# Performance work log

Measured on AMD Instinct MI355X. Metric: run time of the kernel, lower is better.

## Reference

```python
import jax, jax.numpy as jnp
import numpy as np

SEQ, BATCH, EMBED = 2048, 4, 1024
NUM_HEADS = 16
HEAD_DIM = EMBED // NUM_HEADS


def setup_inputs() -> dict:
    key = jax.random.key(0)
    k1, k2, k3 = jax.random.split(key, 3)
    # xavier-ish scaling for weights
    query = jax.random.normal(k1, (SEQ, BATCH, EMBED), dtype=jnp.float32)
    in_proj_weight = jax.random.normal(k2, (3 * EMBED, EMBED), dtype=jnp.float32) * (2.0 / np.sqrt(EMBED + 3 * EMBED))
    out_proj_weight = jax.random.normal(k3, (EMBED, EMBED), dtype=jnp.float32) * (1.0 / np.sqrt(EMBED))
    in_proj_bias = jnp.zeros((3 * EMBED,), dtype=jnp.float32)
    out_proj_bias = jnp.zeros((EMBED,), dtype=jnp.float32)
    return {
        "query": query,
        "in_proj_weight": in_proj_weight,
        "in_proj_bias": in_proj_bias,
        "out_proj_weight": out_proj_weight,
        "out_proj_bias": out_proj_bias,
    }


def reference(query, in_proj_weight, in_proj_bias, out_proj_weight, out_proj_bias):
    T, B, C = query.shape
    H, D = NUM_HEADS, HEAD_DIM
    scaling = 1.0 / jnp.sqrt(jnp.asarray(D, dtype=query.dtype))
    # fused QKV projection: [T,B,C] @ [C,3C] -> [T,B,3C]
    qkv = query @ in_proj_weight.T + in_proj_bias
    q, k, v = jnp.split(qkv, 3, axis=-1)
    q = (q * scaling).reshape(T, B, H, D)
    k = k.reshape(T, B, H, D)
    v = v.reshape(T, B, H, D)
    # scores: [B,H,T,S]
    scores = jnp.einsum("tbhd,sbhd->bhts", q, k)
    probs = jax.nn.softmax(scores, axis=-1)
    # context: [T,B,H,D] -> [T,B,C]
    ctx = jnp.einsum("bhts,sbhd->tbhd", probs, v).reshape(T, B, C)
    out = ctx @ out_proj_weight.T + out_proj_bias
    return out
```

## Files before the change

### kernel.cpp

```cpp
#include <hip/hip_runtime.h>
#include <hip/hip_bf16.h>
#include <stdint.h>

#define SEQ_T 2048
#define NBATCH 4
#define CEMB 1024
#define NH 16
#define DH 64
#define MROWS 8192

typedef short bf16x8 __attribute__((ext_vector_type(8)));
typedef float f32x4 __attribute__((ext_vector_type(4)));
typedef float f32x16 __attribute__((ext_vector_type(16)));
typedef unsigned short u16x8 __attribute__((ext_vector_type(8)));
typedef unsigned int u32x2 __attribute__((ext_vector_type(2)));

__device__ __forceinline__ unsigned short f2bf(float f) {
    union { float f; unsigned u; } v; v.f = f;
    unsigned r = (v.u + 0x7FFFu + ((v.u >> 16) & 1u)) >> 16;
    return (unsigned short)r;
}

__device__ __forceinline__ unsigned bfbits(float f) {
    __hip_bfloat16 h = __float2bfloat16(f);
    unsigned short u;
    __builtin_memcpy(&u, &h, 2);
    return (unsigned)u;
}

__device__ __forceinline__ f32x4 mfma16(bf16x8 a, bf16x8 b, f32x4 c) {
    return __builtin_amdgcn_mfma_f32_16x16x32_bf16(a, b, c, 0, 0, 0);
}
__device__ __forceinline__ f32x16 mfma32(bf16x8 a, bf16x8 b, f32x16 c) {
    return __builtin_amdgcn_mfma_f32_32x32x16_bf16(a, b, c, 0, 0, 0);
}

#define GLL16(g, l) __builtin_amdgcn_global_load_lds( \
    (const __attribute__((address_space(1))) void*)(g), \
    (__attribute__((address_space(3))) void*)(l), 16, 0, 0)

__global__ void cast_f32_bf16(const float* __restrict__ in, unsigned short* __restrict__ out, int n) {
    int i = blockIdx.x * blockDim.x + threadIdx.x;
    int stride = gridDim.x * blockDim.x;
    for (int idx = i * 4; idx < n; idx += stride * 4) {
        float4 f = *reinterpret_cast<const float4*>(in + idx);
        ushort4 o;
        o.x = f2bf(f.x); o.y = f2bf(f.y); o.z = f2bf(f.z); o.w = f2bf(f.w);
        *reinterpret_cast<ushort4*>(out + idx) = o;
    }
}

template<int MODE>
__global__ __launch_bounds__(256)
void gemm_bt(const unsigned short* __restrict__ A,
             const unsigned short* __restrict__ Bw,
             const float* __restrict__ bias,
             unsigned short* __restrict__ oQ,
             unsigned short* __restrict__ oK,
             unsigned short* __restrict__ oV,
             float* __restrict__ oF)
{
    __shared__ unsigned char sA[8192];
    __shared__ unsigned char sB[8192];
    const int tid = threadIdx.x;
    const int wid = tid >> 6, lane = tid & 63;
    const int g = lane >> 4, lr = lane & 15;
    const int wr = wid >> 1, wc = wid & 1;
    const int m0 = blockIdx.y * 128, n0 = blockIdx.x * 128;
    const int K = CEMB;

    f32x4 acc[4][4];
    #pragma unroll
    for (int i = 0; i < 4; i++)
        #pragma unroll
        for (int j = 0; j < 4; j++)
            #pragma unroll
            for (int r = 0; r < 4; r++) acc[i][j][r] = 0.f;

    const char* Ab = (const char*)A;
    const char* Bb = (const char*)Bw;

    for (int k0 = 0; k0 < K; k0 += 32) {
        #pragma unroll
        for (int r2 = 0; r2 < 2; r2++) {
            int o = r2 * 4096 + tid * 16;
            int f = o ^ (((o >> 7) & 3) << 4);
            int row = f >> 6, cb = f & 63;
            GLL16(Ab + (size_t)(m0 + row) * (K * 2) + k0 * 2 + cb, sA + r2 * 4096 + wid * 1024);
            GLL16(Bb + (size_t)(n0 + row) * (K * 2) + k0 * 2 + cb, sB + r2 * 4096 + wid * 1024);
        }
        __syncthreads();
        bf16x8 af[4], bfr[4];
        #pragma unroll
        for (int mi = 0; mi < 4; mi++) {
            int row = wr * 64 + mi * 16 + lr;
            int addr = row * 64 + ((g * 16) ^ (((row >> 1) & 3) << 4));
            af[mi] = *(const bf16x8*)(sA + addr);
        }
        #pragma unroll
        for (int ni = 0; ni < 4; ni++) {
            int row = wc * 64 + ni * 16 + lr;
            int addr = row * 64 + ((g * 16) ^ (((row >> 1) & 3) << 4));
            bfr[ni] = *(const bf16x8*)(sB + addr);
        }
        #pragma unroll
        for (int mi = 0; mi < 4; mi++)
            #pragma unroll
            for (int ni = 0; ni < 4; ni++)
                acc[mi][ni] = mfma16(af[mi], bfr[ni], acc[mi][ni]);
        __syncthreads();
    }

    #pragma unroll
    for (int mi = 0; mi < 4; mi++) {
        #pragma unroll
        for (int ni = 0; ni < 4; ni++) {
            int c = n0 + wc * 64 + ni * 16 + lr;
            float bv = bias[c];
            #pragma unroll
            for (int r = 0; r < 4; r++) {
                int m = m0 + wr * 64 + mi * 16 + g * 4 + r;
                float v = acc[mi][ni][r] + bv;
                if (MODE == 0) {
                    int sec = c >> 10, h = (c >> 6) & 15, d = c & 63;
                    int t = m >> 2, b = m & 3;
                    size_t addr = ((size_t)(b * NH + h) * SEQ_T + t) * DH + d;
                    unsigned short val = f2bf(sec == 0 ? v * (0.125f * 1.44269504f) : v);
                    if (sec == 0) oQ[addr] = val;
                    else if (sec == 1) oK[addr] = val;
                    else oV[addr] = val;
                } else {
                    oF[(size_t)m * CEMB + c] = v;
                }
            }
        }
    }
}

__global__ void vtrans(const unsigned short* __restrict__ V, unsigned short* __restrict__ VT) {
    __shared__ unsigned short tile[64][72];
    const int bh = blockIdx.y, t0 = blockIdx.x * 64;
    const int tid = threadIdx.x;
    const unsigned short* src = V + ((size_t)bh * SEQ_T + t0) * DH;
    #pragma unroll
    for (int r = 0; r < 2; r++) {
        int e = r * 2048 + tid * 8;
        u16x8 v = *(const u16x8*)(src + e);
        int row = e >> 6, col = e & 63;
        *(u16x8*)&tile[row][col] = v;
    }
    __syncthreads();
    unsigned short* dst = VT + (size_t)bh * DH * SEQ_T + t0;
    #pragma unroll
    for (int r = 0; r < 2; r++) {
        int e = r * 2048 + tid * 8;
        int d = e >> 6, tc = e & 63;
        u16x8 o;
        #pragma unroll
        for (int j = 0; j < 8; j++) o[j] = tile[tc + j][d];
        *(u16x8*)(dst + (size_t)d * SEQ_T + tc) = o;
    }
}

__global__ __launch_bounds__(256, 2)
void attn(const unsigned short* __restrict__ Qg,
          const unsigned short* __restrict__ Kg,
          const unsigned short* __restrict__ VTg,
          unsigned short* __restrict__ CTX)
{
    __shared__ unsigned char sKs[2][8192];
    __shared__ unsigned char sVs[2][8192];

    const int id = blockIdx.x;
    const int swz = (id & 7) * 128 + (id >> 3);
    const int bh = swz >> 4, qblk = swz & 15;
    const int q0 = qblk * 128;
    const int tid = threadIdx.x, wid = tid >> 6, lane = tid & 63;
    const int ql = lane & 31, h = lane >> 5;

    const char* Kb = (const char*)(Kg + (size_t)bh * SEQ_T * DH);
    const char* Vb = (const char*)(VTg + (size_t)bh * DH * SEQ_T);
    const unsigned short* Qb = Qg + (size_t)bh * SEQ_T * DH;

    const unsigned short* Qrow = Qb + (size_t)(q0 + wid * 32 + ql) * DH;
    const bf16x8 qf0 = *(const bf16x8*)(Qrow + 0 + h * 8);
    const bf16x8 qf1 = *(const bf16x8*)(Qrow + 16 + h * 8);
    const bf16x8 qf2 = *(const bf16x8*)(Qrow + 32 + h * 8);
    const bf16x8 qf3 = *(const bf16x8*)(Qrow + 48 + h * 8);

    f32x16 ctx0, ctx1;
    #pragma unroll
    for (int r = 0; r < 16; r++) { ctx0[r] = 0.f; ctx1[r] = 0.f; }
    float lrun = 0.f;

    auto stage = [&](int buf, int s0) {
        #pragma unroll
        for (int r2 = 0; r2 < 2; r2++) {
            int o = r2 * 4096 + tid * 16;
            int f = o ^ (((o >> 7) & 7) << 4);
            int row = f >> 7, cb = f & 127;
            GLL16(Kb + (size_t)(s0 + row) * 128 + cb, &sKs[buf][r2 * 4096 + wid * 1024]);
            GLL16(Vb + (size_t)row * (SEQ_T * 2) + s0 * 2 + cb, &sVs[buf][r2 * 4096 + wid * 1024]);
        }
    };

    stage(0, 0);
    __syncthreads();

    const int swk = (ql & 7) << 4;

    int cur = 0;
    for (int tt = 0; tt < SEQ_T / 64; tt++) {
        if (tt + 1 < SEQ_T / 64) stage(cur ^ 1, (tt + 1) * 64);
        const unsigned char* kb = sKs[cur];
        const unsigned char* vbuf = sVs[cur];

        f32x16 S0, S1;
        #pragma unroll
        for (int r = 0; r < 16; r++) { S0[r] = 0.f; S1[r] = 0.f; }

        __builtin_amdgcn_s_setprio(1);
        {
            const unsigned char* kr0 = kb + ql * 128;
            S0 = mfma32(*(const bf16x8*)(kr0 + ((h * 16) ^ swk)), qf0, S0);
            S0 = mfma32(*(const bf16x8*)(kr0 + ((32 + h * 16) ^ swk)), qf1, S0);
            S0 = mfma32(*(const bf16x8*)(kr0 + ((64 + h * 16) ^ swk)), qf2, S0);
            S0 = mfma32(*(const bf16x8*)(kr0 + ((96 + h * 16) ^ swk)), qf3, S0);
            const unsigned char* kr1 = kb + (32 + ql) * 128;
            S1 = mfma32(*(const bf16x8*)(kr1 + ((h * 16) ^ swk)), qf0, S1);
            S1 = mfma32(*(const bf16x8*)(kr1 + ((32 + h * 16) ^ swk)), qf1, S1);
            S1 = mfma32(*(const bf16x8*)(kr1 + ((64 + h * 16) ^ swk)), qf2, S1);
            S1 = mfma32(*(const bf16x8*)(kr1 + ((96 + h * 16) ^ swk)), qf3, S1);
        }
        __builtin_amdgcn_s_setprio(0);

        float p[32];
        #pragma unroll
        for (int r = 0; r < 16; r++) p[r] = exp2f(S0[r]);
        #pragma unroll
        for (int r = 0; r < 16; r++) p[16 + r] = exp2f(S1[r]);

        float rs0 = 0.f, rs1 = 0.f;
        #pragma unroll
        for (int r = 0; r < 32; r += 2) { rs0 += p[r]; rs1 += p[r + 1]; }
        float rs = rs0 + rs1;
        rs += __shfl_xor(rs, 32);
        lrun += rs;

        unsigned pw[16];
        #pragma unroll
        for (int w = 0; w < 16; w++)
            pw[w] = (bfbits(p[2 * w + 1]) << 16) | bfbits(p[2 * w]);

        __builtin_amdgcn_s_setprio(1);
        #pragma unroll
        for (int t = 0; t < 4; t++) {
            union { unsigned u[4]; bf16x8 v; } pa;
            pa.u[0] = pw[4 * t]; pa.u[1] = pw[4 * t + 1];
            pa.u[2] = pw[4 * t + 2]; pa.u[3] = pw[4 * t + 3];
            {
                const unsigned char* vr = vbuf + ql * 128;
                union { unsigned u[4]; bf16x8 v; } vf;
                *(u32x2*)&vf.u[0] = *(const u32x2*)(vr + ((t * 32 + h * 8) ^ swk));
                *(u32x2*)&vf.u[2] = *(const u32x2*)(vr + ((t * 32 + h * 8 + 16) ^ swk));
                ctx0 = mfma32(pa.v, vf.v, ctx0);
            }
            {
                const unsigned char* vr = vbuf + (32 + ql) * 128;
                union { unsigned u[4]; bf16x8 v; } vf;
                *(u32x2*)&vf.u[0] = *(const u32x2*)(vr + ((t * 32 + h * 8) ^ swk));
                *(u32x2*)&vf.u[2] = *(const u32x2*)(vr + ((t * 32 + h * 8 + 16) ^ swk));
                ctx1 = mfma32(pa.v, vf.v, ctx1);
            }
        }
        __builtin_amdgcn_s_setprio(0);

        __syncthreads();
        cur ^= 1;
    }

    const int b = bh >> 4, hh = bh & 15;
    #pragma unroll
    for (int r = 0; r < 16; r++) {
        int qq = (r & 3) + 8 * (r >> 2) + 4 * h;
        float lv = __shfl(lrun, qq);
        float inv = __builtin_amdgcn_rcpf(lv);
        int tg = q0 + wid * 32 + qq;
        size_t rowbase = (size_t)(tg * 4 + b) * CEMB + hh * 64;
        CTX[rowbase + ql] = f2bf(ctx0[r] * inv);
        CTX[rowbase + 32 + ql] = f2bf(ctx1[r] * inv);
    }
}

extern "C" void kernel_launch(void* const* d_in, const int* in_sizes, int n_in,
                              void* d_out, int out_size, void* d_ws, size_t ws_size,
                              hipStream_t stream) {
    const float* query  = (const float*)d_in[0];
    const float* w_in   = (const float*)d_in[1];
    const float* b_in   = (const float*)d_in[2];
    const float* w_out  = (const float*)d_in[3];
    const float* b_out  = (const float*)d_in[4];
    float* out = (float*)d_out;

    char* ws = (char*)d_ws;
    unsigned short* Xbf  = (unsigned short*)(ws);
    unsigned short* Wqkv = (unsigned short*)(ws + 16777216);
    unsigned short* Wout = (unsigned short*)(ws + 23068672);
    unsigned short* Q    = (unsigned short*)(ws + 25165824);
    unsigned short* K    = (unsigned short*)(ws + 41943040);
    unsigned short* V    = (unsigned short*)(ws + 58720256);
    unsigned short* VT   = (unsigned short*)(ws + 75497472);
    unsigned short* CTX  = (unsigned short*)(ws + 92274688);

    cast_f32_bf16<<<4096, 256, 0, stream>>>(query, Xbf, MROWS * CEMB);
    cast_f32_bf16<<<2048, 256, 0, stream>>>(w_in, Wqkv, 3 * CEMB * CEMB);
    cast_f32_bf16<<<1024, 256, 0, stream>>>(w_out, Wout, CEMB * CEMB);

    gemm_bt<0><<<dim3(24, 64), 256, 0, stream>>>(Xbf, Wqkv, b_in, Q, K, V, nullptr);
    vtrans<<<dim3(32, 64), 256, 0, stream>>>(V, VT);
    attn<<<1024, 256, 0, stream>>>(Q, K, VT, CTX);
    gemm_bt<1><<<dim3(8, 64), 256, 0, stream>>>(CTX, Wout, b_out, nullptr, nullptr, nullptr, out);
}
```

Measured before the change: 240.4 us.

## Streamline attention inner loop with raw exp2, packed bf16 cvt, higher occupancy

Replaces exp2f with the hardware v_exp_f32 builtin and the per-element bf16 rounding with a packed v_cvt_pk_bf16_f32 instruction. It also precomputes the LDS and global address offsets once and unrolls the double-buffered loop by two so buffer indices become compile-time constants. The occupancy hint rises from 2 to 4 blocks per CU. These steps cut VALU and address arithmetic per tile, at the risk of register spills under the tighter launch bounds and slightly different exp/rounding precision.

```diff
diff --git a/kernel.cpp b/kernel.cpp
--- a/kernel.cpp
+++ b/kernel.cpp
@@ -21,18 +21,29 @@
     return (unsigned short)r;
 }
 
-__device__ __forceinline__ unsigned bfbits(float f) {
-    __hip_bfloat16 h = __float2bfloat16(f);
-    unsigned short u;
-    __builtin_memcpy(&u, &h, 2);
-    return (unsigned)u;
-}
-
 __device__ __forceinline__ f32x4 mfma16(bf16x8 a, bf16x8 b, f32x4 c) {
     return __builtin_amdgcn_mfma_f32_16x16x32_bf16(a, b, c, 0, 0, 0);
 }
 __device__ __forceinline__ f32x16 mfma32(bf16x8 a, bf16x8 b, f32x16 c) {
     return __builtin_amdgcn_mfma_f32_32x32x16_bf16(a, b, c, 0, 0, 0);
+}
+
+#if defined(__has_builtin)
+#if __has_builtin(__builtin_amdgcn_exp2f)
+#define EXP2(x) __builtin_amdgcn_exp2f(x)
+#endif
+#endif
+#ifndef EXP2
+__device__ __forceinline__ float __exp2_asm(float x) {
+    float r; asm("v_exp_f32 %0, %1" : "=v"(r) : "v"(x)); return r;
+}
+#define EXP2(x) __exp2_asm(x)
+#endif
+
+__device__ __forceinline__ unsigned cvtpk(float lo, float hi) {
+    unsigned r;
+    asm("v_cvt_pk_bf16_f32 %0, %1, %2" : "=v"(r) : "v"(lo), "v"(hi));
+    return r;
 }
 
 #define GLL16(g, l) __builtin_amdgcn_global_load_lds( \
@@ -162,14 +173,14 @@
     }
 }
 
-__global__ __launch_bounds__(256, 2)
+__global__ __launch_bounds__(256, 4)
 void attn(const unsigned short* __restrict__ Qg,
           const unsigned short* __restrict__ Kg,
           const unsigned short* __restrict__ VTg,
           unsigned short* __restrict__ CTX)
 {
-    __shared__ unsigned char sKs[2][8192];
-    __shared__ unsigned char sVs[2][8192];
+    __shared__ unsigned char sK[16384];
+    __shared__ unsigned char sV[16384];
 
     const int id = blockIdx.x;
     const int swz = (id & 7) * 128 + (id >> 3);
@@ -193,90 +204,105 @@
     for (int r = 0; r < 16; r++) { ctx0[r] = 0.f; ctx1[r] = 0.f; }
     float lrun = 0.f;
 
-    auto stage = [&](int buf, int s0) {
-        #pragma unroll
-        for (int r2 = 0; r2 < 2; r2++) {
-            int o = r2 * 4096 + tid * 16;
-            int f = o ^ (((o >> 7) & 7) << 4);
-            int row = f >> 7, cb = f & 127;
-            GLL16(Kb + (size_t)(s0 + row) * 128 + cb, &sKs[buf][r2 * 4096 + wid * 1024]);
-            GLL16(Vb + (size_t)row * (SEQ_T * 2) + s0 * 2 + cb, &sVs[buf][r2 * 4096 + wid * 1024]);
-        }
-    };
-
-    stage(0, 0);
+    const int swk = (ql & 7) << 4;
+    const int kOff0 = ql * 128 + ((0 * 32 + h * 16) ^ swk);
+    const int kOff1 = ql * 128 + ((1 * 32 + h * 16) ^ swk);
+    const int kOff2 = ql * 128 + ((2 * 32 + h * 16) ^ swk);
+    const int kOff3 = ql * 128 + ((3 * 32 + h * 16) ^ swk);
+    int vOffA[4], vOffB[4];
+    #pragma unroll
+    for (int t = 0; t < 4; t++) {
+        vOffA[t] = ql * 128 + ((t * 32 + h * 8) ^ swk);
+        vOffB[t] = ql * 128 + ((t * 32 + h * 8 + 16) ^ swk);
+    }
+
+    int o0 = tid * 16;
+    int f0 = o0 ^ (((o0 >> 7) & 7) << 4);
+    int o1 = 4096 + tid * 16;
+    int f1 = o1 ^ (((o1 >> 7) & 7) << 4);
+    const char* kbase0 = Kb + (size_t)(f0 >> 7) * 128 + (f0 & 127);
+    const char* kbase1 = Kb + (size_t)(f1 >> 7) * 128 + (f1 & 127);
+    const char* vbase0 = Vb + (size_t)(f0 >> 7) * (SEQ_T * 2) + (f0 & 127);
+    const char* vbase1 = Vb + (size_t)(f1 >> 7) * (SEQ_T * 2) + (f1 & 127);
+
+#define STAGE(BUF, S0)                                                       \
+    {                                                                        \
+        GLL16(kbase0 + (size_t)(S0) * 128, sK + (BUF) * 8192 + wid * 1024);  \
+        GLL16(kbase1 + (size_t)(S0) * 128, sK + (BUF) * 8192 + 4096 + wid * 1024); \
+        GLL16(vbase0 + (size_t)(S0) * 2, sV + (BUF) * 8192 + wid * 1024);    \
+        GLL16(vbase1 + (size_t)(S0) * 2, sV + (BUF) * 8192 + 4096 + wid * 1024); \
+    }
+
+#define LD8(p) (*(const bf16x8*)(p))
+
+#define ATTN_TILE(BUF)                                                       \
+    {                                                                        \
+        const unsigned char* kb = sK + (BUF) * 8192;                         \
+        const unsigned char* vb = sV + (BUF) * 8192;                         \
+        f32x16 S0, S1;                                                       \
+        _Pragma("unroll")                                                    \
+        for (int r = 0; r < 16; r++) { S0[r] = 0.f; S1[r] = 0.f; }           \
+        __builtin_amdgcn_s_setprio(1);                                       \
+        S0 = mfma32(LD8(kb + kOff0), qf0, S0);                               \
+        S0 = mfma32(LD8(kb + kOff1), qf1, S0);                               \
+        S0 = mfma32(LD8(kb + kOff2), qf2, S0);                               \
+        S0 = mfma32(LD8(kb + kOff3), qf3, S0);                               \
+        S1 = mfma32(LD8(kb + 4096 + kOff0), qf0, S1);                        \
+        S1 = mfma32(LD8(kb + 4096 + kOff1), qf1, S1);                        \
+        S1 = mfma32(LD8(kb + 4096 + kOff2), qf2, S1);                        \
+        S1 = mfma32(LD8(kb + 4096 + kOff3), qf3, S1);                        \
+        __builtin_amdgcn_s_setprio(0);                                       \
+        _Pragma("unroll")                                                    \
+        for (int r = 0; r < 16; r++) S0[r] = EXP2(S0[r]);                    \
+        _Pragma("unroll")                                                    \
+        for (int r = 0; r < 16; r++) S1[r] = EXP2(S1[r]);                    \
+        float a0 = (S0[0] + S0[1]) + (S0[2] + S0[3]);                        \
+        float a1 = (S0[4] + S0[5]) + (S0[6] + S0[7]);                        \
+        float a2 = (S0[8] + S0[9]) + (S0[10] + S0[11]);                      \
+        float a3 = (S0[12] + S0[13]) + (S0[14] + S0[15]);                    \
+        float b0 = (S1[0] + S1[1]) + (S1[2] + S1[3]);                        \
+        float b1 = (S1[4] + S1[5]) + (S1[6] + S1[7]);                        \
+        float b2 = (S1[8] + S1[9]) + (S1[10] + S1[11]);                      \
+        float b3 = (S1[12] + S1[13]) + (S1[14] + S1[15]);                    \
+        float rs = ((a0 + a1) + (a2 + a3)) + ((b0 + b1) + (b2 + b3));        \
+        rs += __shfl_xor(rs, 32);                                            \
+        lrun += rs;                                                          \
+        unsigned pw[16];                                                     \
+        _Pragma("unroll")                                                    \
+        for (int w = 0; w < 8; w++) pw[w] = cvtpk(S0[2 * w], S0[2 * w + 1]); \
+        _Pragma("unroll")                                                    \
+        for (int w = 0; w < 8; w++) pw[8 + w] = cvtpk(S1[2 * w], S1[2 * w + 1]); \
+        __builtin_amdgcn_s_setprio(1);                                       \
+        _Pragma("unroll")                                                    \
+        for (int t = 0; t < 4; t++) {                                        \
+            union { unsigned u[4]; bf16x8 v; } pa;                           \
+            pa.u[0] = pw[4 * t]; pa.u[1] = pw[4 * t + 1];                    \
+            pa.u[2] = pw[4 * t + 2]; pa.u[3] = pw[4 * t + 3];                \
+            {                                                                \
+                union { unsigned u[4]; bf16x8 v; } vf;                       \
+                *(u32x2*)&vf.u[0] = *(const u32x2*)(vb + vOffA[t]);          \
+                *(u32x2*)&vf.u[2] = *(const u32x2*)(vb + vOffB[t]);          \
+                ctx0 = mfma32(pa.v, vf.v, ctx0);                             \
+            }                                                                \
+            {                                                                \
+                union { unsigned u[4]; bf16x8 v; } vf;                       \
+                *(u32x2*)&vf.u[0] = *(const u32x2*)(vb + 4096 + vOffA[t]);   \
+                *(u32x2*)&vf.u[2] = *(const u32x2*)(vb + 4096 + vOffB[t]);   \
+                ctx1 = mfma32(pa.v, vf.v, ctx1);                             \
+            }                                                                \
+        }                                                                    \
+        __builtin_amdgcn_s_setprio(0);                                       \
+    }
+
+    STAGE(0, 0);
     __syncthreads();
-
-    const int swk = (ql & 7) << 4;
-
-    int cur = 0;
-    for (int tt = 0; tt < SEQ_T / 64; tt++) {
-        if (tt + 1 < SEQ_T / 64) stage(cur ^ 1, (tt + 1) * 64);
-        const unsigned char* kb = sKs[cur];
-        const unsigned char* vbuf = sVs[cur];
-
-        f32x16 S0, S1;
-        #pragma unroll
-        for (int r = 0; r < 16; r++) { S0[r] = 0.f; S1[r] = 0.f; }
-
-        __builtin_amdgcn_s_setprio(1);
-        {
-            const unsigned char* kr0 = kb + ql * 128;
-            S0 = mfma32(*(const bf16x8*)(kr0 + ((h * 16) ^ swk)), qf0, S0);
-            S0 = mfma32(*(const bf16x8*)(kr0 + ((32 + h * 16) ^ swk)), qf1, S0);
-            S0 = mfma32(*(const bf16x8*)(kr0 + ((64 + h * 16) ^ swk)), qf2, S0);
-            S0 = mfma32(*(const bf16x8*)(kr0 + ((96 + h * 16) ^ swk)), qf3, S0);
-            const unsigned char* kr1 = kb + (32 + ql) * 128;
-            S1 = mfma32(*(const bf16x8*)(kr1 + ((h * 16) ^ swk)), qf0, S1);
-            S1 = mfma32(*(const bf16x8*)(kr1 + ((32 + h * 16) ^ swk)), qf1, S1);
-            S1 = mfma32(*(const bf16x8*)(kr1 + ((64 + h * 16) ^ swk)), qf2, S1);
-            S1 = mfma32(*(const bf16x8*)(kr1 + ((96 + h * 16) ^ swk)), qf3, S1);
-        }
-        __builtin_amdgcn_s_setprio(0);
-
-        float p[32];
-        #pragma unroll
-        for (int r = 0; r < 16; r++) p[r] = exp2f(S0[r]);
-        #pragma unroll
-        for (int r = 0; r < 16; r++) p[16 + r] = exp2f(S1[r]);
-
-        float rs0 = 0.f, rs1 = 0.f;
-        #pragma unroll
-        for (int r = 0; r < 32; r += 2) { rs0 += p[r]; rs1 += p[r + 1]; }
-        float rs = rs0 + rs1;
-        rs += __shfl_xor(rs, 32);
-        lrun += rs;
-
-        unsigned pw[16];
-        #pragma unroll
-        for (int w = 0; w < 16; w++)
-            pw[w] = (bfbits(p[2 * w + 1]) << 16) | bfbits(p[2 * w]);
-
-        __builtin_amdgcn_s_setprio(1);
-        #pragma unroll
-        for (int t = 0; t < 4; t++) {
-            union { unsigned u[4]; bf16x8 v; } pa;
-            pa.u[0] = pw[4 * t]; pa.u[1] = pw[4 * t + 1];
-            pa.u[2] = pw[4 * t + 2]; pa.u[3] = pw[4 * t + 3];
-            {
-                const unsigned char* vr = vbuf + ql * 128;
-                union { unsigned u[4]; bf16x8 v; } vf;
-                *(u32x2*)&vf.u[0] = *(const u32x2*)(vr + ((t * 32 + h * 8) ^ swk));
-                *(u32x2*)&vf.u[2] = *(const u32x2*)(vr + ((t * 32 + h * 8 + 16) ^ swk));
-                ctx0 = mfma32(pa.v, vf.v, ctx0);
-            }
-            {
-                const unsigned char* vr = vbuf + (32 + ql) * 128;
-                union { unsigned u[4]; bf16x8 v; } vf;
-                *(u32x2*)&vf.u[0] = *(const u32x2*)(vr + ((t * 32 + h * 8) ^ swk));
-                *(u32x2*)&vf.u[2] = *(const u32x2*)(vr + ((t * 32 + h * 8 + 16) ^ swk));
-                ctx1 = mfma32(pa.v, vf.v, ctx1);
-            }
-        }
-        __builtin_amdgcn_s_setprio(0);
-
+    for (int s0 = 0; s0 < SEQ_T; s0 += 128) {
+        STAGE(1, s0 + 64);
+        ATTN_TILE(0);
         __syncthreads();
-        cur ^= 1;
+        if (s0 + 128 < SEQ_T) STAGE(0, s0 + 128);
+        ATTN_TILE(1);
+        __syncthreads();
     }
 
     const int b = bh >> 4, hh = bh & 15;
@@ -290,6 +316,9 @@
         CTX[rowbase + ql] = f2bf(ctx0[r] * inv);
         CTX[rowbase + 32 + ql] = f2bf(ctx1[r] * inv);
     }
+#undef STAGE
+#undef LD8
+#undef ATTN_TILE
 }
 
 extern "C" void kernel_launch(void* const* d_in, const int* in_sizes, int n_in,
```

After: 256.0 us. 6.5% more time.
